# Performance work log

Hardware: AMD Instinct MI355X
Metric: run time of the kernel (lower is better)

## Reference

```python
import jax, jax.numpy as jnp
import numpy as np
import math

N_HEAD = 16
HEAD_DIM = 32  # n_state // n_head // 2
THETA = 10000.0
LAMBDA_INIT = 0.8 - 0.6 * math.exp(-0.3 * 12)  # depth=12
EPS = 1e-5


def _rope_tables(seq_len):
    inv = 1.0 / (THETA ** (np.arange(0, HEAD_DIM, 2, dtype=np.float32) / HEAD_DIM))  # [hd/2]
    t = np.arange(seq_len, dtype=np.float32)
    freqs = np.outer(t, inv)  # [S, hd/2]
    return jnp.asarray(np.cos(freqs)), jnp.asarray(np.sin(freqs))


def _apply_rope_interleaved(x, cos, sin):
    # x: [B,S,H,D]; cos/sin: [S,D/2]; interleaved pairs (even, odd)
    x1, x2 = x[..., 0::2], x[..., 1::2]
    c = cos[None, :, None, :]
    s = sin[None, :, None, :]
    ye = x1 * c - x2 * s
    yo = x1 * s + x2 * c
    return jnp.stack([ye, yo], axis=-1).reshape(x.shape)


def setup_inputs() -> dict:
    key = jax.random.key(0)
    ks = jax.random.split(key, 10)
    B, S, D = 1, 2048, 1024
    hd = HEAD_DIM
    inp = {
        "x": jax.random.normal(ks[0], (B, S, D), jnp.float32),
        "Wq": jax.random.normal(ks[1], (D, D), jnp.float32) * 0.02,
        "Wk": jax.random.normal(ks[2], (D, D), jnp.float32) * 0.02,
        "Wv": jax.random.normal(ks[3], (D, D), jnp.float32) * 0.02,
        "Wo": jax.random.normal(ks[4], (D, D), jnp.float32) * 0.02,
        "lambda_q1": jax.random.normal(ks[5], (hd,), jnp.float32) * 0.1,
        "lambda_k1": jax.random.normal(ks[6], (hd,), jnp.float32) * 0.1,
        "lambda_q2": jax.random.normal(ks[7], (hd,), jnp.float32) * 0.1,
        "lambda_k2": jax.random.normal(ks[8], (hd,), jnp.float32) * 0.1,
        "gamma": jnp.ones((2 * hd,), jnp.float32),
    }
    return inp


def reference(x, Wq, Wk, Wv, Wo, lambda_q1, lambda_k1, lambda_q2, lambda_k2, gamma):
    B, S, D = x.shape
    H, hd = N_HEAD, HEAD_DIM

    q = x @ Wq.T
    k = x @ Wk.T
    v = x @ Wv.T

    q = q.reshape(B, S, 2 * H, hd)
    k = k.reshape(B, S, 2 * H, hd)
    v = v.reshape(B, S, H, 2, hd)

    cos, sin = _rope_tables(S)
    q = _apply_rope_interleaved(q, cos, sin)
    k = _apply_rope_interleaved(k, cos, sin)

    q = q.reshape(B, S, H, 2, hd)
    k = k.reshape(B, S, H, 2, hd)
    q1, q2 = q[:, :, :, 0], q[:, :, :, 1]
    k1, k2 = k[:, :, :, 0], k[:, :, :, 1]
    v1, v2 = v[:, :, :, 0], v[:, :, :, 1]

    scale = hd ** -0.5
    causal = jnp.tril(jnp.ones((S, S), dtype=bool))
    neg = jnp.finfo(x.dtype).min

    def probs(qh, kh):
        s = jnp.einsum('bihd,bjhd->bhij', qh, kh) * scale
        s = jnp.where(causal[None, None], s, neg)
        return jax.nn.softmax(s, axis=-1)

    p1 = probs(q1, k1)  # reused for v1 and v2 (attn11, attn12)
    a11 = jnp.einsum('bhij,bjhd->bihd', p1, v1)
    a12 = jnp.einsum('bhij,bjhd->bihd', p1, v2)
    attn1 = jnp.concatenate([a11, a12], axis=-1)  # [B,S,H,2hd]

    p2 = probs(q2, k2)
    a21 = jnp.einsum('bhij,bjhd->bihd', p2, v1)
    a22 = jnp.einsum('bhij,bjhd->bihd', p2, v2)
    attn2 = jnp.concatenate([a21, a22], axis=-1)

    lam1 = jnp.exp(jnp.sum(lambda_q1 * lambda_k1))
    lam2 = jnp.exp(jnp.sum(lambda_q2 * lambda_k2))
    lam = lam1 - lam2 + LAMBDA_INIT

    wv = attn1 - lam * attn2
    # RMSNorm over last dim (2*hd) with affine gamma
    wv = wv * jax.lax.rsqrt(jnp.mean(wv * wv, axis=-1, keepdims=True) + EPS) * gamma
    wv = wv * (1.0 - LAMBDA_INIT)

    wv = wv.reshape(B, S, H * 2 * hd)
    return wv @ Wo.T
```

## Files before the change

kernel.cpp:

```cpp
#include <hip/hip_runtime.h>
#include <hip/hip_bf16.h>
#include <math.h>


typedef __bf16 bf16x8 __attribute__((ext_vector_type(8)));
typedef float f32x4 __attribute__((ext_vector_type(4)));
typedef float f32x16 __attribute__((ext_vector_type(16)));

#define LOG2E 1.4426950408889634f
#define SCALE 0.17677669529663687f
#define C1EXP 0.25506100319239545f
#define DMAX_THR 31.36f
#define LAM_INIT 0.783605766532f
#define ONE_M_LI 0.216394233468f

#define GLOAD16(g, l)                                                              \
  __builtin_amdgcn_global_load_lds((const __attribute__((address_space(1))) void*)(g), \
                                   (__attribute__((address_space(3))) void*)(l), 16, 0, 0)

__device__ __forceinline__ ushort f2b(float f) {
  unsigned u = __builtin_bit_cast(unsigned, f);
  u += 0x7fffu + ((u >> 16) & 1u);
  return (ushort)(u >> 16);
}
__device__ __forceinline__ float b2f(ushort h) {
  return __builtin_bit_cast(float, ((unsigned)h) << 16);
}
__device__ __forceinline__ ushort f2h(float f) {
  _Float16 h = (_Float16)f;
  return __builtin_bit_cast(ushort, h);
}
__device__ __forceinline__ float h2f(ushort u) {
  return (float)__builtin_bit_cast(_Float16, u);
}
__device__ __forceinline__ int swz128(int row, int byteoff) {
  return row * 128 + (byteoff ^ ((row & 7) << 4));
}
__device__ __forceinline__ int qoff4(int qt) {
  int G = qt >> 2, rem = qt & 3;
  return 2 * G * (G + 1) + rem * (G + 1);
}
__device__ __forceinline__ f32x16 zero16() {
  f32x16 z;
#pragma unroll
  for (int i = 0; i < 16; ++i) z[i] = 0.f;
  return z;
}
__device__ __forceinline__ float max3(float a, float b, float c) {
  return fmaxf(fmaxf(a, b), c);
}

__global__ __launch_bounds__(256) void prep_kernel(
    const float* __restrict__ x, const float* __restrict__ Wq,
    const float* __restrict__ Wk, const float* __restrict__ Wv,
    const float* __restrict__ Wo,
    ushort* __restrict__ xb, ushort* __restrict__ w1, ushort* __restrict__ wob,
    float* __restrict__ cosT, float* __restrict__ sinT) {
  unsigned b = blockIdx.x;
  if (b < 3072u) {
    unsigned i8 = (b * 256u + threadIdx.x) * 8u;
    const float* s;
    ushort* d;
    if (i8 < 2097152u) { s = x + i8; d = xb + i8; }
    else if (i8 < 3145728u) { s = Wq + (i8 - 2097152u); d = w1 + (i8 - 2097152u); }
    else if (i8 < 4194304u) { s = Wk + (i8 - 3145728u); d = w1 + (i8 - 2097152u); }
    else if (i8 < 5242880u) { s = Wv + (i8 - 4194304u); d = w1 + (i8 - 2097152u); }
    else { s = Wo + (i8 - 5242880u); d = wob + (i8 - 5242880u); }
    float4 v0 = *(const float4*)s;
    float4 v1 = *(const float4*)(s + 4);
    union { ushort h[8]; uint4 u; } o;
    o.h[0] = f2b(v0.x); o.h[1] = f2b(v0.y); o.h[2] = f2b(v0.z); o.h[3] = f2b(v0.w);
    o.h[4] = f2b(v1.x); o.h[5] = f2b(v1.y); o.h[6] = f2b(v1.z); o.h[7] = f2b(v1.w);
    *(uint4*)d = o.u;
    return;
  }
  unsigned j = (b - 3072u) * 256u + threadIdx.x;
  int tt = (int)(j >> 4), jj = (int)(j & 15u);
  float inv = powf(10000.0f, -(float)(2 * jj) * (1.0f / 32.0f));
  float ang = (float)tt * inv;
  cosT[j] = cosf(ang);
  sinT[j] = sinf(ang);
}

__global__ __launch_bounds__(256) void ropetv_kernel(ushort* __restrict__ qkv,
                                                     const float* __restrict__ cosT,
                                                     const float* __restrict__ sinT,
                                                     ushort* __restrict__ vt) {
  __shared__ __align__(16) ushort tile[64][80];
  const int t = threadIdx.x;
  if (blockIdx.x < 2048u) {
    unsigned i = blockIdx.x * 256u + t;
    int row = (int)(i >> 8), u4 = (int)(i & 255u);
    int colbase = (u4 < 128) ? (u4 * 8) : (1024 + (u4 - 128) * 8);
    int pbase = u4 * 4;
    ushort* p = qkv + (size_t)row * 3072 + colbase;
    uint4 v = *(const uint4*)p;
    unsigned vv[4] = {v.x, v.y, v.z, v.w};
    unsigned ov[4];
#pragma unroll
    for (int tpp = 0; tpp < 4; ++tpp) {
      int j = (pbase + tpp) & 15;
      float c = cosT[row * 16 + j], s = sinT[row * 16 + j];
      float x1 = b2f((ushort)(vv[tpp] & 0xffffu));
      float x2 = b2f((ushort)(vv[tpp] >> 16));
      float ye = x1 * c - x2 * s;
      float yo = x1 * s + x2 * c;
      ov[tpp] = (unsigned)f2b(ye) | ((unsigned)f2b(yo) << 16);
    }
    uint4 o = {ov[0], ov[1], ov[2], ov[3]};
    *(uint4*)p = o;
    return;
  }
  const int bb = (int)blockIdx.x - 2048;
  const int d0 = (bb & 15) * 64, s0 = (bb >> 4) * 64;
#pragma unroll
  for (int p = 0; p < 2; ++p) {
    int sl = p * 32 + (t >> 3), d8 = (t & 7) * 8;
    uint4 v = *(const uint4*)(qkv + (size_t)(s0 + sl) * 3072 + 2048 + d0 + d8);
    *(uint4*)(&tile[sl][d8]) = v;
  }
  __syncthreads();
#pragma unroll
  for (int p = 0; p < 2; ++p) {
    int dl = p * 32 + (t >> 3), s8 = (t & 7) * 8;
    union { ushort h[8]; uint4 u; } tmp;
#pragma unroll
    for (int jj = 0; jj < 8; ++jj) tmp.h[jj] = tile[s8 + jj][dl];
    *(uint4*)(vt + (size_t)(d0 + dl) * 2048 + s0 + s8) = tmp.u;
  }
}

template <int BM, int BN>
__global__ __launch_bounds__(256) void gemm_bt(const ushort* __restrict__ A,
                                               const ushort* __restrict__ B,
                                               void* __restrict__ C, int M, int N, int K,
                                               int out_bf16) {
  __shared__ __align__(16) ushort As[BM * 64];
  __shared__ __align__(16) ushort Bs[BN * 64];
  const int t = threadIdx.x, lane = t & 63, w = t >> 6;
  const int g = lane >> 4, r = lane & 15;
  const int wr = w >> 1, wc = w & 1;
  const int m0 = blockIdx.y * BM, n0 = blockIdx.x * BN;
  constexpr int AM = BM / 32, AN = BN / 32;

  f32x4 acc[AM][AN];
#pragma unroll
  for (int i = 0; i < AM; ++i)
#pragma unroll
    for (int j = 0; j < AN; ++j) acc[i][j] = (f32x4){0.f, 0.f, 0.f, 0.f};

  for (int k0 = 0; k0 < K; k0 += 64) {
    __syncthreads();
#pragma unroll
    for (int p = 0; p < BM / 32; ++p) {
      int idx = p * 256 + t;
      int row = idx >> 3;
      int bo = ((idx & 7) * 16) ^ ((row & 7) << 4);
      GLOAD16(A + (size_t)(m0 + row) * K + k0 + (bo >> 1), As + idx * 8);
    }
#pragma unroll
    for (int p = 0; p < BN / 32; ++p) {
      int idx = p * 256 + t;
      int row = idx >> 3;
      int bo = ((idx & 7) * 16) ^ ((row & 7) << 4);
      GLOAD16(B + (size_t)(n0 + row) * K + k0 + (bo >> 1), Bs + idx * 8);
    }
    __syncthreads();
#pragma unroll
    for (int ks = 0; ks < 2; ++ks) {
      bf16x8 af[AM], bfr[AN];
#pragma unroll
      for (int i = 0; i < AM; ++i)
        af[i] = __builtin_bit_cast(bf16x8, *(const uint4*)((const char*)As + swz128(wr * (BM / 2) + i * 16 + r, (ks * 32 + g * 8) * 2)));
#pragma unroll
      for (int i = 0; i < AN; ++i)
        bfr[i] = __builtin_bit_cast(bf16x8, *(const uint4*)((const char*)Bs + swz128(wc * (BN / 2) + i * 16 + r, (ks * 32 + g * 8) * 2)));
#pragma unroll
      for (int mi = 0; mi < AM; ++mi)
#pragma unroll
        for (int ni = 0; ni < AN; ++ni)
          acc[mi][ni] = __builtin_amdgcn_mfma_f32_16x16x32_bf16(af[mi], bfr[ni], acc[mi][ni], 0, 0, 0);
    }
  }
#pragma unroll
  for (int mi = 0; mi < AM; ++mi)
#pragma unroll
    for (int ni = 0; ni < AN; ++ni)
#pragma unroll
      for (int e = 0; e < 4; ++e) {
        int row = m0 + wr * (BM / 2) + mi * 16 + g * 4 + e;
        int col = n0 + wc * (BN / 2) + ni * 16 + r;
        float v = acc[mi][ni][e];
        if (out_bf16) ((ushort*)C)[(size_t)row * N + col] = f2b(v);
        else ((float*)C)[(size_t)row * N + col] = v;
      }
}

#define ATTN_STAGE(kt_, Kb, Vb)                                                         \
  do {                                                                                  \
    _Pragma("unroll") for (int p_ = 0; p_ < 2; ++p_) {                                  \
      int idx_ = (p_ * 4 + w) * 64 + lane;                                              \
      int row_ = idx_ >> 3;                                                             \
      int kbs_ = ((idx_ & 7) * 16) ^ ((row_ & 7) << 4);                                 \
      const ushort* gk_ = qkv + (size_t)((kt_) * 64 + row_) * 3072 + 1024 + h * 64 + (kbs_ >> 1); \
      const ushort* gv_ = vt + (size_t)(h * 64 + row_) * 2048 + (kt_) * 64 + (kbs_ >> 1);         \
      GLOAD16(gk_, (Kb) + (p_ * 4 + w) * 512);                                          \
      GLOAD16(gv_, (Vb) + (p_ * 4 + w) * 512);                                          \
    }                                                                                   \
  } while (0)

__global__ __launch_bounds__(256, 3) void attn_split_kernel(
    const ushort* __restrict__ qkv, const ushort* __restrict__ vt,
    ushort* __restrict__ pOh, float* __restrict__ pML) {
  __shared__ __align__(16) ushort Ks[2][64 * 64];
  __shared__ __align__(16) ushort Vs[2][64 * 64];

  int wi = blockIdx.x, qt = 0, c = 0;
  for (int q = 0; q < 32; ++q) {
    int nc = (q >> 2) + 1;
    if (wi < nc) { qt = q; c = wi; break; }
    wi -= nc;
  }
  const int h = blockIdx.y;
  const int pid = h * 144 + qoff4(qt) + c;
  const int t = threadIdx.x, lane = t & 63, w = t >> 6;
  const int sub = w & 1, qh = w >> 1;
  const int ql = lane & 31, g1 = lane >> 5;
  const int qa = qt * 64 + qh * 32 + ql;

  bf16x8 qf0 = __builtin_bit_cast(bf16x8, *(const uint4*)(qkv + (size_t)qa * 3072 + h * 64 + sub * 32 + g1 * 8));
  bf16x8 qf1 = __builtin_bit_cast(bf16x8, *(const uint4*)(qkv + (size_t)qa * 3072 + h * 64 + sub * 32 + 16 + g1 * 8));

  const int koff0a = swz128(ql, (sub * 32 + g1 * 8) * 2);
  const int koff0b = swz128(32 + ql, (sub * 32 + g1 * 8) * 2);
  const int koff1a = swz128(ql, (sub * 32 + 16 + g1 * 8) * 2);
  const int koff1b = swz128(32 + ql, (sub * 32 + 16 + g1 * 8) * 2);
  int voffa[4], voffb[4];
#pragma unroll
  for (int ks = 0; ks < 4; ++ks) {
    voffa[ks] = swz128(ql, (ks * 16 + g1 * 8) * 2);
    voffb[ks] = swz128(32 + ql, (ks * 16 + g1 * 8) * 2);
  }

  f32x16 O0 = zero16(), O1 = zero16();
  float mm = -1e30f, lsum = 0.f;

  auto do_tile = [&](int kt, const ushort* Ksb, const ushort* Vsb) {
    const char* Kc = (const char*)Ksb;
    const char* Vc = (const char*)Vsb;

    f32x16 s0 = zero16(), s1 = zero16();
    {
      bf16x8 ka = __builtin_bit_cast(bf16x8, *(const uint4*)(Kc + koff0a));
      bf16x8 kb = __builtin_bit_cast(bf16x8, *(const uint4*)(Kc + koff0b));
      bf16x8 kc = __builtin_bit_cast(bf16x8, *(const uint4*)(Kc + koff1a));
      bf16x8 kd = __builtin_bit_cast(bf16x8, *(const uint4*)(Kc + koff1b));
      __builtin_amdgcn_s_setprio(1);
      s0 = __builtin_amdgcn_mfma_f32_32x32x16_bf16(ka, qf0, s0, 0, 0, 0);
      s1 = __builtin_amdgcn_mfma_f32_32x32x16_bf16(kb, qf0, s1, 0, 0, 0);
      s0 = __builtin_amdgcn_mfma_f32_32x32x16_bf16(kc, qf1, s0, 0, 0, 0);
      s1 = __builtin_amdgcn_mfma_f32_32x32x16_bf16(kd, qf1, s1, 0, 0, 0);
      __builtin_amdgcn_s_setprio(0);
    }

    if (kt == qt) {
      const int lim = qh * 32 + ql;
#pragma unroll
      for (int rg = 0; rg < 16; ++rg) {
        int kv0 = (rg & 3) + 4 * g1 + 8 * (rg >> 2);
        if (kv0 > lim) s0[rg] = -1e30f;
        if (kv0 + 32 > lim) s1[rg] = -1e30f;
      }
    }

    float a0 = max3(s0[0], s0[1], s0[2]);
    float a1 = max3(s0[3], s0[4], s0[5]);
    float a2 = max3(s0[6], s0[7], s0[8]);
    float a3 = max3(s0[9], s0[10], s0[11]);
    float a4 = max3(s0[12], s0[13], s0[14]);
    float b0 = max3(s1[0], s1[1], s1[2]);
    float b1 = max3(s1[3], s1[4], s1[5]);
    float b2 = max3(s1[6], s1[7], s1[8]);
    float b3 = max3(s1[9], s1[10], s1[11]);
    float b4 = max3(s1[12], s1[13], s1[14]);
    float c0 = max3(a0, a1, a2);
    float c1 = max3(a3, a4, s0[15]);
    float c2 = max3(b0, b1, b2);
    float c3 = max3(b3, b4, s1[15]);
    float rm = fmaxf(max3(c0, c1, c2), c3);
    rm = fmaxf(rm, __shfl_xor(rm, 32));

    if (!__all(rm - mm <= DMAX_THR)) {
      float mn = fmaxf(mm, rm);
      float es = exp2f((mm - mn) * C1EXP);
      mm = mn;
      lsum *= es;
      O0 *= es;
      O1 *= es;
    }

    const float mnC = mm * C1EXP;
    float pa = 0.f, pb = 0.f, pc = 0.f, pd = 0.f;
#pragma unroll
    for (int rg = 0; rg < 16; rg += 2) {
      float p00 = exp2f(__builtin_fmaf(s0[rg], C1EXP, -mnC));
      float p01 = exp2f(__builtin_fmaf(s0[rg + 1], C1EXP, -mnC));
      float p10 = exp2f(__builtin_fmaf(s1[rg], C1EXP, -mnC));
      float p11 = exp2f(__builtin_fmaf(s1[rg + 1], C1EXP, -mnC));
      s0[rg] = p00; s0[rg + 1] = p01;
      s1[rg] = p10; s1[rg + 1] = p11;
      pa += p00; pb += p01; pc += p10; pd += p11;
    }
    float ps = (pa + pb) + (pc + pd);
    ps += __shfl_xor(ps, 32);
    lsum += ps;

    unsigned pk[2][4][2];
#pragma unroll
    for (int q2 = 0; q2 < 4; ++q2) {
      float x0 = s0[4 * q2 + 0], x1 = s0[4 * q2 + 1], x2 = s0[4 * q2 + 2], x3 = s0[4 * q2 + 3];
      float y0 = s1[4 * q2 + 0], y1 = s1[4 * q2 + 1], y2 = s1[4 * q2 + 2], y3 = s1[4 * q2 + 3];
      asm("v_cvt_pk_bf16_f32 %0, %1, %2" : "=v"(pk[0][q2][0]) : "v"(x0), "v"(x1));
      asm("v_cvt_pk_bf16_f32 %0, %1, %2" : "=v"(pk[0][q2][1]) : "v"(x2), "v"(x3));
      asm("v_cvt_pk_bf16_f32 %0, %1, %2" : "=v"(pk[1][q2][0]) : "v"(y0), "v"(y1));
      asm("v_cvt_pk_bf16_f32 %0, %1, %2" : "=v"(pk[1][q2][1]) : "v"(y2), "v"(y3));
    }
#pragma unroll
    for (int kvb = 0; kvb < 2; ++kvb) {
      asm volatile("v_permlane32_swap_b32 %0, %1" : "+v"(pk[kvb][0][0]), "+v"(pk[kvb][1][0]));
      asm volatile("v_permlane32_swap_b32 %0, %1" : "+v"(pk[kvb][0][1]), "+v"(pk[kvb][1][1]));
      asm volatile("v_permlane32_swap_b32 %0, %1" : "+v"(pk[kvb][2][0]), "+v"(pk[kvb][3][0]));
      asm volatile("v_permlane32_swap_b32 %0, %1" : "+v"(pk[kvb][2][1]), "+v"(pk[kvb][3][1]));
    }

#pragma unroll
    for (int ks = 0; ks < 4; ++ks) {
      const int kvb = ks >> 1, kshi = ks & 1;
      uint4 pu;
      pu.x = pk[kvb][2 * kshi][0];
      pu.y = pk[kvb][2 * kshi][1];
      pu.z = pk[kvb][2 * kshi + 1][0];
      pu.w = pk[kvb][2 * kshi + 1][1];
      bf16x8 pf = __builtin_bit_cast(bf16x8, pu);
      bf16x8 v0 = __builtin_bit_cast(bf16x8, *(const uint4*)(Vc + voffa[ks]));
      bf16x8 v1 = __builtin_bit_cast(bf16x8, *(const uint4*)(Vc + voffb[ks]));
      __builtin_amdgcn_s_setprio(1);
      O0 = __builtin_amdgcn_mfma_f32_32x32x16_bf16(v0, pf, O0, 0, 0, 0);
      O1 = __builtin_amdgcn_mfma_f32_32x32x16_bf16(v1, pf, O1, 0, 0, 0);
      __builtin_amdgcn_s_setprio(0);
    }
  };

  const int ktb = c * 4;
  const int kte = min(ktb + 4, qt + 1);
  for (int kt0 = ktb; kt0 < kte; kt0 += 2) {
    const bool two = (kt0 + 1 < kte);
    __syncthreads();
    ATTN_STAGE(kt0, Ks[0], Vs[0]);
    if (two) ATTN_STAGE(kt0 + 1, Ks[1], Vs[1]);
    __syncthreads();
    do_tile(kt0, Ks[0], Vs[0]);
    if (two) do_tile(kt0 + 1, Ks[1], Vs[1]);
  }

  const int qrow = qh * 32 + ql;
  float* pml = pML + (size_t)pid * 256 + sub * 128;
  if (g1 == 0) {
    pml[qrow] = mm;
    pml[64 + qrow] = lsum;
  }
  ushort* po = pOh + ((size_t)(pid * 2 + sub) * 64 + qrow) * 64;
#pragma unroll
  for (int q2 = 0; q2 < 4; ++q2) {
    uint2 u0, u1;
    u0.x = (unsigned)f2h(O0[4 * q2 + 0]) | ((unsigned)f2h(O0[4 * q2 + 1]) << 16);
    u0.y = (unsigned)f2h(O0[4 * q2 + 2]) | ((unsigned)f2h(O0[4 * q2 + 3]) << 16);
    u1.x = (unsigned)f2h(O1[4 * q2 + 0]) | ((unsigned)f2h(O1[4 * q2 + 1]) << 16);
    u1.y = (unsigned)f2h(O1[4 * q2 + 2]) | ((unsigned)f2h(O1[4 * q2 + 3]) << 16);
    *(uint2*)(po + q2 * 8 + g1 * 4) = u0;
    *(uint2*)(po + 32 + q2 * 8 + g1 * 4) = u1;
  }
}

__global__ __launch_bounds__(256) void combine_kernel(
    const ushort* __restrict__ pOh, const float* __restrict__ pML,
    const float* __restrict__ lq1, const float* __restrict__ lk1,
    const float* __restrict__ lq2, const float* __restrict__ lk2,
    const float* __restrict__ gamma, ushort* __restrict__ attn_out) {
  const int qt = blockIdx.x, h = blockIdx.y;
  const int nc = (qt >> 2) + 1;
  const int pbase = h * 144 + qoff4(qt);
  const int t = threadIdx.x, row = t >> 2, quad = t & 3;
  const int lane = t & 63;

  float lam;
  {
    int d = lane & 31;
    float a1 = lq1[d] * lk1[d];
    float a2 = lq2[d] * lk2[d];
#pragma unroll
    for (int m = 16; m >= 1; m >>= 1) {
      a1 += __shfl_xor(a1, m);
      a2 += __shfl_xor(a2, m);
    }
    lam = expf(a1) - expf(a2) + LAM_INIT;
  }

  float M[2] = {-1e30f, -1e30f};
  for (int c = 0; c < nc; ++c) {
    const float* ml = pML + (size_t)(pbase + c) * 256;
    M[0] = fmaxf(M[0], ml[row]);
    M[1] = fmaxf(M[1], ml[128 + row]);
  }
  float L[2] = {0.f, 0.f};
  float acc[2][16];
#pragma unroll
  for (int s = 0; s < 2; ++s)
#pragma unroll
    for (int v = 0; v < 16; ++v) acc[s][v] = 0.f;

  for (int c = 0; c < nc; ++c) {
    const int pid = pbase + c;
    const float* ml = pML + (size_t)pid * 256;
#pragma unroll
    for (int s = 0; s < 2; ++s) {
      float mc = ml[s * 128 + row];
      float lc = ml[s * 128 + 64 + row];
      float wgt = exp2f((mc - M[s]) * C1EXP);
      L[s] += lc * wgt;
      const ushort* op = pOh + ((size_t)(pid * 2 + s) * 64 + row) * 64 + quad * 16;
      uint4 ua = *(const uint4*)op;
      uint4 ub = *(const uint4*)(op + 8);
      unsigned uu[8] = {ua.x, ua.y, ua.z, ua.w, ub.x, ub.y, ub.z, ub.w};
#pragma unroll
      for (int j = 0; j < 8; ++j) {
        acc[s][2 * j + 0] += h2f((ushort)(uu[j] & 0xffffu)) * wgt;
        acc[s][2 * j + 1] += h2f((ushort)(uu[j] >> 16)) * wgt;
      }
    }
  }

  float inv0 = 1.f / L[0], inv1 = 1.f / L[1];
  float wv[16], ss = 0.f;
#pragma unroll
  for (int j = 0; j < 16; ++j) {
    float val = acc[0][j] * inv0 - lam * (acc[1][j] * inv1);
    wv[j] = val;
    ss += val * val;
  }
  ss += __shfl_xor(ss, 1);
  ss += __shfl_xor(ss, 2);
  float scl = rsqrtf(ss * (1.f / 64.f) + 1e-5f) * ONE_M_LI;

  union { ushort hs[16]; uint4 u[2]; } outp;
#pragma unroll
  for (int j = 0; j < 16; ++j)
    outp.hs[j] = f2b(wv[j] * scl * gamma[quad * 16 + j]);
  uint4* dst = (uint4*)(attn_out + (size_t)(qt * 64 + row) * 1024 + h * 64 + quad * 16);
  dst[0] = outp.u[0];
  dst[1] = outp.u[1];
}

extern "C" void kernel_launch(void* const* d_in, const int* in_sizes, int n_in,
                              void* d_out, int out_size, void* d_ws, size_t ws_size,
                              hipStream_t stream) {
  const float* x = (const float*)d_in[0];
  const float* Wq = (const float*)d_in[1];
  const float* Wk = (const float*)d_in[2];
  const float* Wv = (const float*)d_in[3];
  const float* Wo = (const float*)d_in[4];
  const float* lq1 = (const float*)d_in[5];
  const float* lk1 = (const float*)d_in[6];
  const float* lq2 = (const float*)d_in[7];
  const float* lk2 = (const float*)d_in[8];
  const float* gamma = (const float*)d_in[9];
  (void)in_sizes; (void)n_in; (void)out_size; (void)ws_size;

  char* ws = (char*)d_ws;
  ushort* xb = (ushort*)(ws);
  ushort* w1 = (ushort*)(ws + (4ull << 20));
  ushort* wob = (ushort*)(ws + (10ull << 20));
  ushort* qkv = (ushort*)(ws + (12ull << 20));
  ushort* vt = (ushort*)(ws + (24ull << 20));
  ushort* atn = (ushort*)(ws + (28ull << 20));
  float* cosT = (float*)(ws + (32ull << 20));
  float* sinT = (float*)(ws + (32ull << 20) + 2048 * 16 * 4);
  const size_t pO_off = (33ull << 20);
  const size_t pml_off = pO_off + 2304ull * 2 * 64 * 64 * 2;
  ushort* pOh = (ushort*)(ws + pO_off);
  float* pML = (float*)(ws + pml_off);

  prep_kernel<<<3200, 256, 0, stream>>>(x, Wq, Wk, Wv, Wo, xb, w1, wob, cosT, sinT);
  gemm_bt<64, 128><<<dim3(24, 32), 256, 0, stream>>>(xb, w1, (void*)qkv, 2048, 3072, 1024, 1);
  ropetv_kernel<<<2560, 256, 0, stream>>>(qkv, cosT, sinT, vt);
  attn_split_kernel<<<dim3(144, 16), 256, 0, stream>>>(qkv, vt, pOh, pML);
  combine_kernel<<<dim3(32, 16), 256, 0, stream>>>(pOh, pML, lq1, lk1, lq2, lk2, gamma, atn);
  gemm_bt<64, 64><<<dim3(16, 32), 256, 0, stream>>>(atn, wob, d_out, 2048, 1024, 1024, 0);
}
```

Baseline: 97.76 us.

## Fuse RoPE into QKV GEMM epilogue and remap blocks across XCDs

Applies the interleaved RoPE rotation inside the QKV GEMM epilogue, pairing even and odd columns with a lane shuffle, so the separate read-modify-write pass over Q and K is removed and the leftover kernel only transposes V. It also remaps block IDs in the GEMM and the attention kernel so that consecutive tiles are grouped per XCD (stride-8 interleave), aiming at better L2 reuse. RoPE is now applied to the fp32 accumulator before the bf16 rounding, which changes rounding slightly, and the epilogue performs extra cos/sin table loads.

```diff
diff --git a/kernel.cpp b/kernel.cpp
--- a/kernel.cpp
+++ b/kernel.cpp
@@ -82,36 +82,11 @@
   sinT[j] = sinf(ang);
 }
 
-__global__ __launch_bounds__(256) void ropetv_kernel(ushort* __restrict__ qkv,
-                                                     const float* __restrict__ cosT,
-                                                     const float* __restrict__ sinT,
+__global__ __launch_bounds__(256) void transv_kernel(const ushort* __restrict__ qkv,
                                                      ushort* __restrict__ vt) {
   __shared__ __align__(16) ushort tile[64][80];
   const int t = threadIdx.x;
-  if (blockIdx.x < 2048u) {
-    unsigned i = blockIdx.x * 256u + t;
-    int row = (int)(i >> 8), u4 = (int)(i & 255u);
-    int colbase = (u4 < 128) ? (u4 * 8) : (1024 + (u4 - 128) * 8);
-    int pbase = u4 * 4;
-    ushort* p = qkv + (size_t)row * 3072 + colbase;
-    uint4 v = *(const uint4*)p;
-    unsigned vv[4] = {v.x, v.y, v.z, v.w};
-    unsigned ov[4];
-#pragma unroll
-    for (int tpp = 0; tpp < 4; ++tpp) {
-      int j = (pbase + tpp) & 15;
-      float c = cosT[row * 16 + j], s = sinT[row * 16 + j];
-      float x1 = b2f((ushort)(vv[tpp] & 0xffffu));
-      float x2 = b2f((ushort)(vv[tpp] >> 16));
-      float ye = x1 * c - x2 * s;
-      float yo = x1 * s + x2 * c;
-      ov[tpp] = (unsigned)f2b(ye) | ((unsigned)f2b(yo) << 16);
-    }
-    uint4 o = {ov[0], ov[1], ov[2], ov[3]};
-    *(uint4*)p = o;
-    return;
-  }
-  const int bb = (int)blockIdx.x - 2048;
+  const int bb = (int)blockIdx.x;
   const int d0 = (bb & 15) * 64, s0 = (bb >> 4) * 64;
 #pragma unroll
   for (int p = 0; p < 2; ++p) {
@@ -130,17 +105,22 @@
   }
 }
 
-template <int BM, int BN>
+template <int BM, int BN, int ROPE>
 __global__ __launch_bounds__(256) void gemm_bt(const ushort* __restrict__ A,
                                                const ushort* __restrict__ B,
                                                void* __restrict__ C, int M, int N, int K,
-                                               int out_bf16) {
+                                               int out_bf16,
+                                               const float* __restrict__ cosT,
+                                               const float* __restrict__ sinT) {
   __shared__ __align__(16) ushort As[BM * 64];
   __shared__ __align__(16) ushort Bs[BN * 64];
   const int t = threadIdx.x, lane = t & 63, w = t >> 6;
   const int g = lane >> 4, r = lane & 15;
   const int wr = w >> 1, wc = w & 1;
-  const int m0 = blockIdx.y * BM, n0 = blockIdx.x * BN;
+  const int nbx = gridDim.x, nwg = gridDim.x * gridDim.y;
+  int bid = blockIdx.x + nbx * blockIdx.y;
+  if ((nwg & 7) == 0) bid = (bid & 7) * (nwg >> 3) + (bid >> 3);
+  const int m0 = (bid / nbx) * BM, n0 = (bid % nbx) * BN;
   constexpr int AM = BM / 32, AN = BN / 32;
 
   f32x4 acc[AM][AN];
@@ -182,18 +162,26 @@
           acc[mi][ni] = __builtin_amdgcn_mfma_f32_16x16x32_bf16(af[mi], bfr[ni], acc[mi][ni], 0, 0, 0);
     }
   }
+  const bool do_rope = ROPE && (n0 < 2048);
 #pragma unroll
   for (int mi = 0; mi < AM; ++mi)
 #pragma unroll
-    for (int ni = 0; ni < AN; ++ni)
+    for (int ni = 0; ni < AN; ++ni) {
+      const int jj = ((ni * 16 + r) & 31) >> 1;
 #pragma unroll
       for (int e = 0; e < 4; ++e) {
         int row = m0 + wr * (BM / 2) + mi * 16 + g * 4 + e;
         int col = n0 + wc * (BN / 2) + ni * 16 + r;
         float v = acc[mi][ni][e];
+        if (do_rope) {
+          float pr = __shfl_xor(v, 1);
+          float cc = cosT[row * 16 + jj], sn = sinT[row * 16 + jj];
+          v = (r & 1) ? (pr * sn + v * cc) : (v * cc - pr * sn);
+        }
         if (out_bf16) ((ushort*)C)[(size_t)row * N + col] = f2b(v);
         else ((float*)C)[(size_t)row * N + col] = v;
       }
+    }
 }
 
 #define ATTN_STAGE(kt_, Kb, Vb)                                                         \
@@ -215,13 +203,14 @@
   __shared__ __align__(16) ushort Ks[2][64 * 64];
   __shared__ __align__(16) ushort Vs[2][64 * 64];
 
-  int wi = blockIdx.x, qt = 0, c = 0;
+  const int id2 = (blockIdx.x & 7) * 288 + (blockIdx.x >> 3);
+  const int h = id2 / 144;
+  int wi = id2 % 144, qt = 0, c = 0;
   for (int q = 0; q < 32; ++q) {
     int nc = (q >> 2) + 1;
     if (wi < nc) { qt = q; c = wi; break; }
     wi -= nc;
   }
-  const int h = blockIdx.y;
   const int pid = h * 144 + qoff4(qt) + c;
   const int t = threadIdx.x, lane = t & 63, w = t >> 6;
   const int sub = w & 1, qh = w >> 1;
@@ -491,9 +480,9 @@
   float* pML = (float*)(ws + pml_off);
 
   prep_kernel<<<3200, 256, 0, stream>>>(x, Wq, Wk, Wv, Wo, xb, w1, wob, cosT, sinT);
-  gemm_bt<64, 128><<<dim3(24, 32), 256, 0, stream>>>(xb, w1, (void*)qkv, 2048, 3072, 1024, 1);
-  ropetv_kernel<<<2560, 256, 0, stream>>>(qkv, cosT, sinT, vt);
-  attn_split_kernel<<<dim3(144, 16), 256, 0, stream>>>(qkv, vt, pOh, pML);
+  gemm_bt<64, 128, 1><<<dim3(24, 32), 256, 0, stream>>>(xb, w1, (void*)qkv, 2048, 3072, 1024, 1, cosT, sinT);
+  transv_kernel<<<512, 256, 0, stream>>>(qkv, vt);
+  attn_split_kernel<<<2304, 256, 0, stream>>>(qkv, vt, pOh, pML);
   combine_kernel<<<dim3(32, 16), 256, 0, stream>>>(pOh, pML, lq1, lk1, lq2, lk2, gamma, atn);
-  gemm_bt<64, 64><<<dim3(16, 32), 256, 0, stream>>>(atn, wob, d_out, 2048, 1024, 1024, 0);
-}
+  gemm_bt<64, 64, 0><<<dim3(16, 32), 256, 0, stream>>>(atn, wob, d_out, 2048, 1024, 1024, 0, nullptr, nullptr);
+}
```

Measured after the change: 99.67 us. No clear change (+2.0%).
